# Performance work log

Hardware: AMD Instinct MI355X
Metric: run time of the kernel (lower is better)

The kernel has to match this reference:

```python
import jax, jax.numpy as jnp
import numpy as np

VOCAB = 32000
BATCH = 256
SEQ = 2048


def setup_inputs() -> dict:
    key = jax.random.key(0)
    docs = jax.random.randint(key, (BATCH, SEQ), 0, VOCAB)  # int32 token ids
    return {"docs": docs}


def reference(docs):
    # Equivalent to mean(one_hot(docs, VOCAB), axis=-2) but computed as a
    # normalized histogram via scatter-add -- never materializes the
    # [B, S, V] one-hot tensor.
    B, S = docs.shape
    rows = jnp.arange(B)[:, None]  # [B, 1] broadcast against [B, S] tokens
    hist = jnp.zeros((B, VOCAB), dtype=jnp.float32).at[rows, docs].add(1.0)
    return hist / jnp.float32(S)
```

## Files before the change

kernel.cpp:

```cpp
#include <hip/hip_runtime.h>


#define VOCAB 32000
#define BATCH 256
#define SEQ   2048
#define NCHUNK 4
#define CHUNK (VOCAB / NCHUNK)
#define BLK   512

typedef float f32x4 __attribute__((ext_vector_type(4)));

__global__ __launch_bounds__(BLK) void bow_hist_kernel(
    const int* __restrict__ docs, float* __restrict__ out) {
    __shared__ unsigned int bins[CHUNK];

    const int wg   = blockIdx.x;
    const int b    = wg >> 2;
    const int c    = wg & (NCHUNK - 1);
    const int base = c * CHUNK;
    const int tid  = threadIdx.x;

    uint4* bins4 = reinterpret_cast<uint4*>(bins);
    for (int i = tid; i < CHUNK / 4; i += BLK) {
        bins4[i] = make_uint4(0u, 0u, 0u, 0u);
    }
    __syncthreads();

    const int4* row4 = reinterpret_cast<const int4*>(docs + (size_t)b * SEQ);
    int4 t = row4[tid];
    int r;
    r = t.x - base; if ((unsigned)r < (unsigned)CHUNK) atomicAdd(&bins[r], 1u);
    r = t.y - base; if ((unsigned)r < (unsigned)CHUNK) atomicAdd(&bins[r], 1u);
    r = t.z - base; if ((unsigned)r < (unsigned)CHUNK) atomicAdd(&bins[r], 1u);
    r = t.w - base; if ((unsigned)r < (unsigned)CHUNK) atomicAdd(&bins[r], 1u);
    __syncthreads();

    float* orow = out + (size_t)b * VOCAB + base;
    const float inv = 1.0f / (float)SEQ;
    for (int i = tid; i < CHUNK / 4; i += BLK) {
        uint4 u = bins4[i];
        f32x4 v;
        v.x = (float)u.x * inv;
        v.y = (float)u.y * inv;
        v.z = (float)u.z * inv;
        v.w = (float)u.w * inv;
        __builtin_nontemporal_store(v, reinterpret_cast<f32x4*>(orow) + i);
    }
}

extern "C" void kernel_launch(void* const* d_in, const int* in_sizes, int n_in,
                              void* d_out, int out_size, void* d_ws, size_t ws_size,
                              hipStream_t stream) {
    const int* docs = (const int*)d_in[0];
    float* out = (float*)d_out;
    bow_hist_kernel<<<dim3(BATCH * NCHUNK), dim3(BLK), 0, stream>>>(docs, out);
}
```

Baseline: 11.30 us.

## Process two batch rows per workgroup with double-buffered smaller vocab chunks

```diff
diff --git a/kernel.cpp b/kernel.cpp
--- a/kernel.cpp
+++ b/kernel.cpp
@@ -4,7 +4,7 @@
 #define VOCAB 32000
 #define BATCH 256
 #define SEQ   2048
-#define NCHUNK 4
+#define NCHUNK 8
 #define CHUNK (VOCAB / NCHUNK)
 #define BLK   512
 
@@ -12,39 +12,70 @@
 
 __global__ __launch_bounds__(BLK) void bow_hist_kernel(
     const int* __restrict__ docs, float* __restrict__ out) {
-    __shared__ unsigned int bins[CHUNK];
+    __shared__ unsigned int bins[2][CHUNK];
 
     const int wg   = blockIdx.x;
-    const int b    = wg >> 2;
     const int c    = wg & (NCHUNK - 1);
+    const int b0   = (wg >> 3) << 1;
     const int base = c * CHUNK;
     const int tid  = threadIdx.x;
 
-    uint4* bins4 = reinterpret_cast<uint4*>(bins);
-    for (int i = tid; i < CHUNK / 4; i += BLK) {
-        bins4[i] = make_uint4(0u, 0u, 0u, 0u);
+    const int4* rA = reinterpret_cast<const int4*>(docs + (size_t)b0 * SEQ);
+    const int4* rB = reinterpret_cast<const int4*>(docs + (size_t)(b0 + 1) * SEQ);
+    int4 tA = rA[tid];
+    int4 tB = rB[tid];
+
+    uint4* buf0 = reinterpret_cast<uint4*>(bins[0]);
+    uint4* buf1 = reinterpret_cast<uint4*>(bins[1]);
+    const float inv = 1.0f / (float)SEQ;
+
+    for (int i = tid; i < CHUNK / 4; i += BLK) buf0[i] = make_uint4(0u, 0u, 0u, 0u);
+    __syncthreads();
+
+    {
+        int r;
+        r = tA.x - base; if ((unsigned)r < (unsigned)CHUNK) atomicAdd(&bins[0][r], 1u);
+        r = tA.y - base; if ((unsigned)r < (unsigned)CHUNK) atomicAdd(&bins[0][r], 1u);
+        r = tA.z - base; if ((unsigned)r < (unsigned)CHUNK) atomicAdd(&bins[0][r], 1u);
+        r = tA.w - base; if ((unsigned)r < (unsigned)CHUNK) atomicAdd(&bins[0][r], 1u);
     }
     __syncthreads();
 
-    const int4* row4 = reinterpret_cast<const int4*>(docs + (size_t)b * SEQ);
-    int4 t = row4[tid];
-    int r;
-    r = t.x - base; if ((unsigned)r < (unsigned)CHUNK) atomicAdd(&bins[r], 1u);
-    r = t.y - base; if ((unsigned)r < (unsigned)CHUNK) atomicAdd(&bins[r], 1u);
-    r = t.z - base; if ((unsigned)r < (unsigned)CHUNK) atomicAdd(&bins[r], 1u);
-    r = t.w - base; if ((unsigned)r < (unsigned)CHUNK) atomicAdd(&bins[r], 1u);
+    {
+        float* o = out + (size_t)b0 * VOCAB + base;
+        for (int i = tid; i < CHUNK / 4; i += BLK) {
+            uint4 u = buf0[i];
+            f32x4 v;
+            v.x = (float)u.x * inv;
+            v.y = (float)u.y * inv;
+            v.z = (float)u.z * inv;
+            v.w = (float)u.w * inv;
+            __builtin_nontemporal_store(v, reinterpret_cast<f32x4*>(o) + i);
+        }
+        for (int i = tid; i < CHUNK / 4; i += BLK) buf1[i] = make_uint4(0u, 0u, 0u, 0u);
+    }
     __syncthreads();
 
-    float* orow = out + (size_t)b * VOCAB + base;
-    const float inv = 1.0f / (float)SEQ;
-    for (int i = tid; i < CHUNK / 4; i += BLK) {
-        uint4 u = bins4[i];
-        f32x4 v;
-        v.x = (float)u.x * inv;
-        v.y = (float)u.y * inv;
-        v.z = (float)u.z * inv;
-        v.w = (float)u.w * inv;
-        __builtin_nontemporal_store(v, reinterpret_cast<f32x4*>(orow) + i);
+    {
+        int r;
+        r = tB.x - base; if ((unsigned)r < (unsigned)CHUNK) atomicAdd(&bins[1][r], 1u);
+        r = tB.y - base; if ((unsigned)r < (unsigned)CHUNK) atomicAdd(&bins[1][r], 1u);
+        r = tB.z - base; if ((unsigned)r < (unsigned)CHUNK) atomicAdd(&bins[1][r], 1u);
+        r = tB.w - base; if ((unsigned)r < (unsigned)CHUNK) atomicAdd(&bins[1][r], 1u);
+    }
+    __syncthreads();
+
+    {
+        float* o = out + (size_t)(b0 + 1) * VOCAB + base;
+        for (int i = tid; i < CHUNK / 4; i += BLK) {
+            uint4 u = buf1[i];
+            f32x4 v;
+            v.x = (float)u.x * inv;
+            v.y = (float)u.y * inv;
+            v.z = (float)u.z * inv;
+            v.w = (float)u.w * inv;
+            __builtin_nontemporal_store(v, reinterpret_cast<f32x4*>(o) + i);
+        }
     }
 }
 
@@ -53,5 +84,5 @@
                               hipStream_t stream) {
     const int* docs = (const int*)d_in[0];
     float* out = (float*)d_out;
-    bow_hist_kernel<<<dim3(BATCH * NCHUNK), dim3(BLK), 0, stream>>>(docs, out);
+    bow_hist_kernel<<<dim3(BATCH * NCHUNK / 2), dim3(BLK), 0, stream>>>(docs, out);
 }
```

Result: slower. 12.76 us (+12.9%).
